# Kernel tuning notes

Hardware: AMD Instinct MI355X
Metric: run time of the kernel (lower is better)

Reference implementation:

```python
import jax, jax.numpy as jnp
import numpy as np

NUM_LEVELS = 4
NUM_CODES = 1024
EMBED_DIM = 256
B, T = 16, 2048


def setup_inputs() -> dict:
    key = jax.random.key(0)
    k1, k2 = jax.random.split(key)
    x = jax.random.normal(k1, (B, T, EMBED_DIM), dtype=jnp.float32)
    # original init: uniform(-1/num_codes, 1/num_codes)
    u = jax.random.uniform(k2, (NUM_LEVELS, NUM_CODES, EMBED_DIM), dtype=jnp.float32)
    codebooks = (u * 2.0 - 1.0) / NUM_CODES
    return {"x": x, "codebooks": codebooks}


def _vq_level(residual_flat, cb):
    # residual_flat: [N, D], cb: [K, D]
    # squared L2 distances: ||r||^2 + ||c||^2 - 2 r.c  -> [N, K]
    dists = (
        jnp.sum(residual_flat ** 2, axis=1, keepdims=True)
        + jnp.sum(cb ** 2, axis=1)
        - 2.0 * residual_flat @ cb.T
    )
    idx = jnp.argmin(dists, axis=1)  # [N]
    quant = cb[idx]  # [N, D] gather
    return quant, idx


def reference(x, codebooks):
    sg = jax.lax.stop_gradient
    shape = x.shape
    D = shape[-1]
    L = codebooks.shape[0]
    residual = x
    total_quant = jnp.zeros_like(x)
    total_q_loss = jnp.float32(0.0)
    total_e_loss = jnp.float32(0.0)
    all_indices = []
    for lvl in range(L):
        flat = residual.reshape(-1, D)
        quant_flat, idx = _vq_level(flat, codebooks[lvl])
        quant = quant_flat.reshape(shape)
        total_q_loss = total_q_loss + jnp.mean((quant - sg(residual)) ** 2)
        total_e_loss = total_e_loss + jnp.mean((sg(quant) - residual) ** 2)
        total_quant = total_quant + quant
        all_indices.append(idx.reshape(shape[:-1]))
        residual = residual - sg(quant)
    quantized_ste = x + sg(total_quant - x)
    q_loss = total_q_loss / L
    e_loss = total_e_loss / L
    indices = jnp.stack(all_indices, axis=0)  # [L, B, T]
    return quantized_ste, q_loss, e_loss, indices
```

## Files before the change

### kernel.cpp

```cpp
#include <hip/hip_runtime.h>

#define NROWS 32768
#define DIM 256
#define KCODES 1024
#define NLEV 4
#define CAP 64
#define MARGIN 8e-3f

typedef short short8v __attribute__((ext_vector_type(8)));
typedef float f32x4v  __attribute__((ext_vector_type(4)));

static __device__ __forceinline__ unsigned short f2bf(float f) {
  unsigned u = __float_as_uint(f);
  unsigned lsb = (u >> 16) & 1u;
  u += 0x7fffu + lsb;
  return (unsigned short)(u >> 16);
}


__global__ __launch_bounds__(256) void k_bnorm(const float* __restrict__ cb,
                                               float* __restrict__ bv) {
  int r = blockIdx.x * blockDim.x + threadIdx.x;
  if (r >= NLEV * KCODES) return;
  const float4* p = reinterpret_cast<const float4*>(cb + (size_t)r * DIM);
  float s0 = 0.f, s1 = 0.f, s2 = 0.f, s3 = 0.f;
  for (int g = 0; g < DIM / 4; ++g) {
    float4 v = p[g];
    s0 += v.x * v.x; s1 += v.y * v.y; s2 += v.z * v.z; s3 += v.w * v.w;
  }
  bv[r] = (s0 + s1) + (s2 + s3);
}

__global__ __launch_bounds__(256) void k_csplit(const float* __restrict__ cb,
                                                unsigned short* __restrict__ chi) {
  const int tid = threadIdx.x;
  const int cr = blockIdx.x * 16 + (tid >> 4);
  const int l16 = tid & 15;
  const float4* p = reinterpret_cast<const float4*>(cb + (size_t)cr * DIM + l16 * 16);
  unsigned w[8];
  #pragma unroll
  for (int j = 0; j < 4; ++j) {
    float4 v = p[j];
    w[2 * j + 0] = (unsigned)f2bf(v.x) | ((unsigned)f2bf(v.y) << 16);
    w[2 * j + 1] = (unsigned)f2bf(v.z) | ((unsigned)f2bf(v.w) << 16);
  }
  const int lvl_ = cr >> 10;
  const int c = cr & 1023;
  unsigned short* base = chi + (size_t)lvl_ * (KCODES * DIM) + (size_t)(c >> 4) * 4096;
  const int c8 = c & 15;
  const int ks = l16 >> 1;
  const int kb0 = (l16 & 1) * 2;
  *reinterpret_cast<uint4*>(base + ks * 512 + kb0 * 128 + c8 * 8) =
      make_uint4(w[0], w[1], w[2], w[3]);
  *reinterpret_cast<uint4*>(base + ks * 512 + (kb0 + 1) * 128 + c8 * 8) =
      make_uint4(w[4], w[5], w[6], w[7]);
}

__global__ __launch_bounds__(256) void k_prep(const float* __restrict__ x,
                                              unsigned short* __restrict__ rhi,
                                              float* __restrict__ rowsq) {
  __shared__ float sred[256];
  const int tid = threadIdx.x;
  const int rr = tid >> 4;
  const int l16 = tid & 15;
  const int row = blockIdx.x * 16 + rr;
  const float4* p = reinterpret_cast<const float4*>(x + (size_t)row * DIM + l16 * 16);
  float e = 0.f;
  unsigned w[8];
  #pragma unroll
  for (int j = 0; j < 4; ++j) {
    float4 v = p[j];
    e += v.x * v.x + v.y * v.y + v.z * v.z + v.w * v.w;
    w[2 * j + 0] = (unsigned)f2bf(v.x) | ((unsigned)f2bf(v.y) << 16);
    w[2 * j + 1] = (unsigned)f2bf(v.z) | ((unsigned)f2bf(v.w) << 16);
  }
  unsigned short* base = rhi + (size_t)blockIdx.x * 4096;
  const int ks = l16 >> 1;
  const int kb0 = (l16 & 1) * 2;
  *reinterpret_cast<uint4*>(base + ks * 512 + kb0 * 128 + rr * 8) =
      make_uint4(w[0], w[1], w[2], w[3]);
  *reinterpret_cast<uint4*>(base + ks * 512 + (kb0 + 1) * 128 + rr * 8) =
      make_uint4(w[4], w[5], w[6], w[7]);
  sred[tid] = e;
  __syncthreads();
  if (tid < 16) {
    float s = 0.f;
    #pragma unroll
    for (int k = 0; k < 16; ++k) s += sred[tid * 16 + k];
    rowsq[blockIdx.x * 16 + tid] = s;
  }
}

__global__ __launch_bounds__(512, 4) void k_screen(const unsigned short* __restrict__ rhi,
                                                   const unsigned short* __restrict__ chi_l,
                                                   const float* __restrict__ bv_l,
                                                   const float* __restrict__ rowsq,
                                                   unsigned* __restrict__ survq,
                                                   unsigned* __restrict__ counts) {
  __shared__ float minb[32][8];
  __shared__ float rowminf[32];
  __shared__ unsigned cnt[32];
  const int tid = threadIdx.x;
  const int lane = tid & 63;
  const int w = tid >> 6;
  const int rb = blockIdx.x;
  const int row0 = rb * 32;
  const int c0 = w * 128;
  const int ln = lane & 15;
  const int kb = lane >> 4;

  f32x4v acc[2][8];
  #pragma unroll
  for (int r = 0; r < 2; ++r)
    #pragma unroll
    for (int t = 0; t < 8; ++t) acc[r][t] = (f32x4v){0.f, 0.f, 0.f, 0.f};

  const unsigned short* pa = rhi + (size_t)(rb * 2) * 4096 + lane * 8;
  const unsigned short* pb = chi_l + (size_t)(w * 8) * 4096 + lane * 8;

  #pragma unroll 1
  for (int ks = 0; ks < 8; ++ks) {
    short8v a0 = *reinterpret_cast<const short8v*>(pa + ks * 512);
    short8v a1 = *reinterpret_cast<const short8v*>(pa + 4096 + ks * 512);
    short8v b0 = *reinterpret_cast<const short8v*>(pb + 0 * 4096 + ks * 512);
    short8v b1 = *reinterpret_cast<const short8v*>(pb + 1 * 4096 + ks * 512);
    short8v b2 = *reinterpret_cast<const short8v*>(pb + 2 * 4096 + ks * 512);
    short8v b3 = *reinterpret_cast<const short8v*>(pb + 3 * 4096 + ks * 512);
    short8v b4 = *reinterpret_cast<const short8v*>(pb + 4 * 4096 + ks * 512);
    short8v b5 = *reinterpret_cast<const short8v*>(pb + 5 * 4096 + ks * 512);
    short8v b6 = *reinterpret_cast<const short8v*>(pb + 6 * 4096 + ks * 512);
    short8v b7 = *reinterpret_cast<const short8v*>(pb + 7 * 4096 + ks * 512);
    __builtin_amdgcn_sched_barrier(0);
    acc[0][0] = __builtin_amdgcn_mfma_f32_16x16x32_bf16(a0, b0, acc[0][0], 0, 0, 0);
    acc[1][0] = __builtin_amdgcn_mfma_f32_16x16x32_bf16(a1, b0, acc[1][0], 0, 0, 0);
    acc[0][1] = __builtin_amdgcn_mfma_f32_16x16x32_bf16(a0, b1, acc[0][1], 0, 0, 0);
    acc[1][1] = __builtin_amdgcn_mfma_f32_16x16x32_bf16(a1, b1, acc[1][1], 0, 0, 0);
    acc[0][2] = __builtin_amdgcn_mfma_f32_16x16x32_bf16(a0, b2, acc[0][2], 0, 0, 0);
    acc[1][2] = __builtin_amdgcn_mfma_f32_16x16x32_bf16(a1, b2, acc[1][2], 0, 0, 0);
    acc[0][3] = __builtin_amdgcn_mfma_f32_16x16x32_bf16(a0, b3, acc[0][3], 0, 0, 0);
    acc[1][3] = __builtin_amdgcn_mfma_f32_16x16x32_bf16(a1, b3, acc[1][3], 0, 0, 0);
    acc[0][4] = __builtin_amdgcn_mfma_f32_16x16x32_bf16(a0, b4, acc[0][4], 0, 0, 0);
    acc[1][4] = __builtin_amdgcn_mfma_f32_16x16x32_bf16(a1, b4, acc[1][4], 0, 0, 0);
    acc[0][5] = __builtin_amdgcn_mfma_f32_16x16x32_bf16(a0, b5, acc[0][5], 0, 0, 0);
    acc[1][5] = __builtin_amdgcn_mfma_f32_16x16x32_bf16(a1, b5, acc[1][5], 0, 0, 0);
    acc[0][6] = __builtin_amdgcn_mfma_f32_16x16x32_bf16(a0, b6, acc[0][6], 0, 0, 0);
    acc[1][6] = __builtin_amdgcn_mfma_f32_16x16x32_bf16(a1, b6, acc[1][6], 0, 0, 0);
    acc[0][7] = __builtin_amdgcn_mfma_f32_16x16x32_bf16(a0, b7, acc[0][7], 0, 0, 0);
    acc[1][7] = __builtin_amdgcn_mfma_f32_16x16x32_bf16(a1, b7, acc[1][7], 0, 0, 0);
  }

  float bvl[8];
  #pragma unroll
  for (int t = 0; t < 8; ++t) bvl[t] = bv_l[c0 + t * 16 + ln];
  float rq[2][4];
  #pragma unroll
  for (int r = 0; r < 2; ++r)
    #pragma unroll
    for (int g = 0; g < 4; ++g) rq[r][g] = rowsq[row0 + r * 16 + kb * 4 + g];

  #pragma unroll
  for (int r = 0; r < 2; ++r) {
    #pragma unroll
    for (int g = 0; g < 4; ++g) {
      float v = __builtin_inff();
      #pragma unroll
      for (int t = 0; t < 8; ++t) {
        float dd = (rq[r][g] + bvl[t]) - 2.0f * acc[r][t][g];
        v = fminf(v, dd);
      }
      #pragma unroll
      for (int m = 1; m < 16; m <<= 1) v = fminf(v, __shfl_xor(v, m));
      if (ln == 0) minb[r * 16 + kb * 4 + g][w] = v;
    }
  }
  __syncthreads();
  if (tid < 32) {
    float v = minb[tid][0];
    #pragma unroll
    for (int k = 1; k < 8; ++k) v = fminf(v, minb[tid][k]);
    rowminf[tid] = v;
    cnt[tid] = 0;
  }
  __syncthreads();
  #pragma unroll
  for (int r = 0; r < 2; ++r) {
    #pragma unroll
    for (int g = 0; g < 4; ++g) {
      const int rowloc = r * 16 + kb * 4 + g;
      const float thr = rowminf[rowloc] + MARGIN;
      #pragma unroll
      for (int t = 0; t < 8; ++t) {
        float dd = (rq[r][g] + bvl[t]) - 2.0f * acc[r][t][g];
        if (dd <= thr) {
          unsigned slot = atomicAdd(&cnt[rowloc], 1u);
          if (slot < CAP)
            survq[(size_t)(row0 + rowloc) * CAP + slot] =
                (unsigned)(c0 + t * 16 + ln);
        }
      }
    }
  }
  __syncthreads();
  if (tid < 32) counts[row0 + tid] = cnt[tid];
}

__global__ __launch_bounds__(256) void k_exupd(const float* __restrict__ x,
                                               const float* __restrict__ cb,
                                               const float* __restrict__ bv,
                                               const float* __restrict__ rowsq,
                                               const unsigned* __restrict__ survq,
                                               const unsigned* __restrict__ counts,
                                               int* __restrict__ idxh,
                                               float* __restrict__ fidx,
                                               float* __restrict__ part,
                                               float* __restrict__ rowsq_o,
                                               unsigned short* __restrict__ rhi,
                                               int lvl) {
  __shared__ __align__(16) float rlds[16][260];
  __shared__ int idsh[16];
  __shared__ float sred[256];
  __shared__ float rsum[16];

  const int tid = threadIdx.x;
  const int rr = tid >> 4;
  const int l16 = tid & 15;
  const int row = blockIdx.x * 16 + rr;
  const size_t obase = (size_t)row * DIM + l16 * 16;
  const float* cb_l = cb + (size_t)lvl * KCODES * DIM;
  const float* bv_l = bv + lvl * KCODES;

  float4 rj[4];
  {
    const float4* xp = reinterpret_cast<const float4*>(x + obase);
    #pragma unroll
    for (int j = 0; j < 4; ++j) rj[j] = xp[j];
    for (int p = 0; p < lvl; ++p) {
      const float4* qp = reinterpret_cast<const float4*>(
          cb + ((size_t)p * KCODES + idxh[p * NROWS + row]) * DIM + l16 * 16);
      #pragma unroll
      for (int j = 0; j < 4; ++j) {
        float4 q = qp[j];
        rj[j].x -= q.x; rj[j].y -= q.y; rj[j].z -= q.z; rj[j].w -= q.w;
      }
    }
    #pragma unroll
    for (int j = 0; j < 4; ++j)
      *reinterpret_cast<float4*>(&rlds[rr][l16 * 16 + 4 * j]) = rj[j];
  }
  __syncthreads();

  const float A = rowsq[row];
  const unsigned n = counts[row];
  unsigned long long best = ~0ull;

#define CHAIN(CODE)                                                            \
  {                                                                            \
    const float* cp2 = cb_l + (size_t)(CODE) * DIM;                            \
    float a0 = 0.f;                                                            \
    _Pragma("unroll 8")                                                        \
    for (int dv = 0; dv < DIM / 4; ++dv) {                                     \
      float4 rv = *reinterpret_cast<const float4*>(&rlds[rr][dv * 4]);         \
      float4 cv = *reinterpret_cast<const float4*>(cp2 + dv * 4);              \
      a0 = fmaf(rv.x, cv.x, a0); a0 = fmaf(rv.y, cv.y, a0);                    \
      a0 = fmaf(rv.z, cv.z, a0); a0 = fmaf(rv.w, cv.w, a0);                    \
    }                                                                          \
    float t = A + bv_l[(CODE)];                                 \
    float dd = t - 2.0f * a0;                  \
    unsigned long long pk =                                                    \
        ((unsigned long long)__float_as_uint(dd) << 32) | (unsigned)(CODE);    \
    best = (pk < best) ? pk : best;                                            \
  }

  if (n <= CAP) {
    for (unsigned s = l16; s < n; s += 16) {
      unsigned code = survq[(size_t)row * CAP + s];
      CHAIN(code);
    }
  } else {
    for (unsigned c = l16; c < KCODES; c += 16) CHAIN(c);
  }
#undef CHAIN

  #pragma unroll
  for (int m = 1; m < 16; m <<= 1) {
    unsigned long long o = __shfl_xor(best, m);
    best = (o < best) ? o : best;
  }
  if (l16 == 0) {
    const int id = (int)(best & 0xffffffffull);
    idxh[lvl * NROWS + row] = id;
    fidx[lvl * NROWS + row] = (float)id;
    idsh[rr] = id;
  }
  __syncthreads();

  const int id = idsh[rr];
  const float4* cpc = reinterpret_cast<const float4*>(
      cb_l + (size_t)id * DIM + l16 * 16);
  float nn[16];
  float e = 0.f;
  #pragma unroll
  for (int j = 0; j < 4; ++j) {
    float4 c = cpc[j];
    float n0 = rj[j].x - c.x, n1 = rj[j].y - c.y;
    float n2 = rj[j].z - c.z, n3 = rj[j].w - c.w;
    nn[4 * j + 0] = n0; nn[4 * j + 1] = n1; nn[4 * j + 2] = n2; nn[4 * j + 3] = n3;
    e += (n0 * n0 + n1 * n1) + (n2 * n2 + n3 * n3);
  }

  if (lvl < 3) {
    unsigned w[8];
    #pragma unroll
    for (int k = 0; k < 8; ++k)
      w[k] = (unsigned)f2bf(nn[2 * k]) | ((unsigned)f2bf(nn[2 * k + 1]) << 16);
    unsigned short* base = rhi + (size_t)blockIdx.x * 4096;
    const int ks = l16 >> 1;
    const int kb0 = (l16 & 1) * 2;
    *reinterpret_cast<uint4*>(base + ks * 512 + kb0 * 128 + rr * 8) =
        make_uint4(w[0], w[1], w[2], w[3]);
    *reinterpret_cast<uint4*>(base + ks * 512 + (kb0 + 1) * 128 + rr * 8) =
        make_uint4(w[4], w[5], w[6], w[7]);
  }

  sred[tid] = e;
  __syncthreads();
  if (tid < 16) {
    float s = 0.f;
    #pragma unroll
    for (int k = 0; k < 16; ++k) s += sred[tid * 16 + k];
    rsum[tid] = s;
    if (lvl < 3) rowsq_o[blockIdx.x * 16 + tid] = s;
  }
  __syncthreads();
  if (tid == 0) {
    float p = 0.f;
    #pragma unroll
    for (int k = 0; k < 16; ++k) p += rsum[k];
    part[blockIdx.x] = p;
  }
}

__global__ __launch_bounds__(256) void k_ste(const float* __restrict__ x,
                                             const float* __restrict__ cb,
                                             const int* __restrict__ idxh,
                                             float* __restrict__ out) {
  const int tid = threadIdx.x;
  const int row = blockIdx.x * 16 + (tid >> 4);
  const int l16 = tid & 15;
  const size_t obase = (size_t)row * DIM + l16 * 16;
  const float4* c0p = reinterpret_cast<const float4*>(
      cb + ((size_t)0 * KCODES + idxh[0 * NROWS + row]) * DIM + l16 * 16);
  const float4* c1p = reinterpret_cast<const float4*>(
      cb + ((size_t)1 * KCODES + idxh[1 * NROWS + row]) * DIM + l16 * 16);
  const float4* c2p = reinterpret_cast<const float4*>(
      cb + ((size_t)2 * KCODES + idxh[2 * NROWS + row]) * DIM + l16 * 16);
  const float4* c3p = reinterpret_cast<const float4*>(
      cb + ((size_t)3 * KCODES + idxh[3 * NROWS + row]) * DIM + l16 * 16);
  const float4* xp = reinterpret_cast<const float4*>(x + obase);
  float4* op = reinterpret_cast<float4*>(out + obase);
  #pragma unroll
  for (int j = 0; j < 4; ++j) {
    float4 c0 = c0p[j], c1 = c1p[j], c2 = c2p[j], c3 = c3p[j], xv = xp[j];
    float4 tv;
    tv.x = c0.x; tv.y = c0.y; tv.z = c0.z; tv.w = c0.w;
    tv.x += c1.x; tv.y += c1.y; tv.z += c1.z; tv.w += c1.w;
    tv.x += c2.x; tv.y += c2.y; tv.z += c2.z; tv.w += c2.w;
    tv.x += c3.x; tv.y += c3.y; tv.z += c3.z; tv.w += c3.w;
    tv.x = xv.x + (tv.x - xv.x); tv.y = xv.y + (tv.y - xv.y);
    tv.z = xv.z + (tv.z - xv.z); tv.w = xv.w + (tv.w - xv.w);
    op[j] = tv;
  }
}

__global__ __launch_bounds__(256) void k_loss(const float* __restrict__ part,
                                              float* __restrict__ out) {
  __shared__ float s[256];
  const int tid = threadIdx.x;
  float means[4];
  for (int l = 0; l < 4; ++l) {
    float sum = 0.f;
    for (int i = tid; i < 2048; i += 256) sum += part[l * 2048 + i];
    s[tid] = sum;
    __syncthreads();
    for (int st = 128; st > 0; st >>= 1) {
      if (tid < st) s[tid] += s[tid + st];
      __syncthreads();
    }
    means[l] = s[0] * (1.0f / 8388608.0f);
    __syncthreads();
  }
  if (tid == 0) {
    float t = ((means[0] + means[1]) + means[2]) + means[3];
    float loss = t * 0.25f;
    out[0] = loss;
    out[1] = loss;
  }
}

extern "C" void kernel_launch(void* const* d_in, const int* in_sizes, int n_in,
                              void* d_out, int out_size, void* d_ws, size_t ws_size,
                              hipStream_t stream) {
  const float* x  = (const float*)d_in[0];
  const float* cb = (const float*)d_in[1];
  float* out = (float*)d_out;
  float* ws  = (float*)d_ws;

  unsigned short* rhi = (unsigned short*)ws;
  unsigned short* chi = (unsigned short*)(ws + 4194304);
  unsigned* survq  = (unsigned*)(ws + 4194304 + 524288);
  unsigned* counts = (unsigned*)(ws + 4194304 + 524288 + 2097152);
  int* idxh = (int*)(ws + 4194304 + 524288 + 2097152 + 131072);
  float* bv    = ws + 4194304 + 524288 + 2097152 + 131072 + 131072;
  float* rowsq = bv + 4096;
  float* part  = rowsq + 32768;

  float* lossout = out + 8388608;
  float* fidx    = out + 8388610;

  k_bnorm<<<16, 256, 0, stream>>>(cb, bv);
  k_csplit<<<256, 256, 0, stream>>>(cb, chi);
  k_prep<<<2048, 256, 0, stream>>>(x, rhi, rowsq);

  for (int l = 0; l < NLEV; ++l) {
    k_screen<<<1024, 512, 0, stream>>>(rhi, chi + (size_t)l * KCODES * DIM,
                                       bv + l * KCODES, rowsq, survq, counts);
    k_exupd<<<2048, 256, 0, stream>>>(x, cb, bv, rowsq, survq, counts,
                                      idxh, fidx, part + l * 2048,
                                      rowsq, rhi, l);
  }

  k_ste<<<2048, 256, 0, stream>>>(x, cb, idxh, out);
  k_loss<<<1, 256, 0, stream>>>(part, lossout);
}
```

Measured before the change: 348.3 us.

## Retile screen kernel to 128 rows by 256 codes with global survivor counters

Each screening block now covers 128 residual rows against a quarter of the codebook, with four row groups by two code halves per block. Before, each block covered 32 rows against all 1024 codes. This shrinks the codebook slice each block streams and raises reuse of the loaded row and code tiles. The per-row threshold now uses the minimum over the block's own 256 codes rather than all codes. Survivor counts move to per-level global atomics zeroed by a memset. The looser local threshold can let more candidates through, adding exact-rescoring work and raising the risk of overflowing the 64-slot cap, and the global atomics add contention.

```diff
diff --git a/kernel.cpp b/kernel.cpp
--- a/kernel.cpp
+++ b/kernel.cpp
@@ -96,16 +96,17 @@
                                                    const float* __restrict__ bv_l,
                                                    const float* __restrict__ rowsq,
                                                    unsigned* __restrict__ survq,
-                                                   unsigned* __restrict__ counts) {
-  __shared__ float minb[32][8];
-  __shared__ float rowminf[32];
-  __shared__ unsigned cnt[32];
+                                                   unsigned* __restrict__ counts_l) {
+  __shared__ float minb[128][2];
   const int tid = threadIdx.x;
   const int lane = tid & 63;
   const int w = tid >> 6;
-  const int rb = blockIdx.x;
-  const int row0 = rb * 32;
-  const int c0 = w * 128;
+  const int rg = w >> 1;
+  const int ch = w & 1;
+  const int rb = blockIdx.x & 255;
+  const int q = blockIdx.x >> 8;
+  const int row0 = rb * 128 + rg * 32;
+  const int c0 = q * 256 + ch * 128;
   const int ln = lane & 15;
   const int kb = lane >> 4;
 
@@ -115,8 +116,8 @@
     #pragma unroll
     for (int t = 0; t < 8; ++t) acc[r][t] = (f32x4v){0.f, 0.f, 0.f, 0.f};
 
-  const unsigned short* pa = rhi + (size_t)(rb * 2) * 4096 + lane * 8;
-  const unsigned short* pb = chi_l + (size_t)(w * 8) * 4096 + lane * 8;
+  const unsigned short* pa = rhi + (size_t)(rb * 8 + rg * 2) * 4096 + lane * 8;
+  const unsigned short* pb = chi_l + (size_t)(q * 16 + ch * 8) * 4096 + lane * 8;
 
   #pragma unroll 1
   for (int ks = 0; ks < 8; ++ks) {
@@ -170,38 +171,28 @@
       }
       #pragma unroll
       for (int m = 1; m < 16; m <<= 1) v = fminf(v, __shfl_xor(v, m));
-      if (ln == 0) minb[r * 16 + kb * 4 + g][w] = v;
+      if (ln == 0) minb[rg * 32 + r * 16 + kb * 4 + g][ch] = v;
     }
   }
   __syncthreads();
-  if (tid < 32) {
-    float v = minb[tid][0];
-    #pragma unroll
-    for (int k = 1; k < 8; ++k) v = fminf(v, minb[tid][k]);
-    rowminf[tid] = v;
-    cnt[tid] = 0;
-  }
-  __syncthreads();
   #pragma unroll
   for (int r = 0; r < 2; ++r) {
     #pragma unroll
     for (int g = 0; g < 4; ++g) {
-      const int rowloc = r * 16 + kb * 4 + g;
-      const float thr = rowminf[rowloc] + MARGIN;
+      const int rowloc = rg * 32 + r * 16 + kb * 4 + g;
+      const int row = rb * 128 + rowloc;
+      const float thr = fminf(minb[rowloc][0], minb[rowloc][1]) + MARGIN;
       #pragma unroll
       for (int t = 0; t < 8; ++t) {
         float dd = (rq[r][g] + bvl[t]) - 2.0f * acc[r][t][g];
         if (dd <= thr) {
-          unsigned slot = atomicAdd(&cnt[rowloc], 1u);
+          unsigned slot = atomicAdd(&counts_l[row], 1u);
           if (slot < CAP)
-            survq[(size_t)(row0 + rowloc) * CAP + slot] =
-                (unsigned)(c0 + t * 16 + ln);
+            survq[(size_t)row * CAP + slot] = (unsigned)(c0 + t * 16 + ln);
         }
       }
     }
   }
-  __syncthreads();
-  if (tid < 32) counts[row0 + tid] = cnt[tid];
 }
 
 __global__ __launch_bounds__(256) void k_exupd(const float* __restrict__ x,
@@ -407,8 +398,8 @@
 
   unsigned short* rhi = (unsigned short*)ws;
   unsigned short* chi = (unsigned short*)(ws + 4194304);
-  unsigned* survq  = (unsigned*)(ws + 4194304 + 524288);
-  unsigned* counts = (unsigned*)(ws + 4194304 + 524288 + 2097152);
+  unsigned* survq   = (unsigned*)(ws + 4194304 + 524288);
+  unsigned* counts4 = (unsigned*)(ws + 4194304 + 524288 + 2097152);
   int* idxh = (int*)(ws + 4194304 + 524288 + 2097152 + 131072);
   float* bv    = ws + 4194304 + 524288 + 2097152 + 131072 + 131072;
   float* rowsq = bv + 4096;
@@ -417,14 +408,16 @@
   float* lossout = out + 8388608;
   float* fidx    = out + 8388610;
 
+  hipMemsetAsync(counts4, 0, (size_t)NLEV * NROWS * sizeof(unsigned), stream);
   k_bnorm<<<16, 256, 0, stream>>>(cb, bv);
   k_csplit<<<256, 256, 0, stream>>>(cb, chi);
   k_prep<<<2048, 256, 0, stream>>>(x, rhi, rowsq);
 
   for (int l = 0; l < NLEV; ++l) {
+    unsigned* counts_l = counts4 + (size_t)l * NROWS;
     k_screen<<<1024, 512, 0, stream>>>(rhi, chi + (size_t)l * KCODES * DIM,
-                                       bv + l * KCODES, rowsq, survq, counts);
-    k_exupd<<<2048, 256, 0, stream>>>(x, cb, bv, rowsq, survq, counts,
+                                       bv + l * KCODES, rowsq, survq, counts_l);
+    k_exupd<<<2048, 256, 0, stream>>>(x, cb, bv, rowsq, survq, counts_l,
                                       idxh, fidx, part + l * 2048,
                                       rowsq, rhi, l);
   }
```

Measured after the change: 634.3 us. 82.1% more time.
